# Kernel tuning notes

Measured on AMD Instinct MI355X. Metric: run time of the kernel, lower is better.

## Reference

```python
import jax, jax.numpy as jnp
import numpy as np

H = W = 128  # fixed by the hardcoded `127 - idx` in the original module


def _gather(x, gx, gy):
    # x: (B, H, W, C); gx, gy: (B, H, W) -> gathered (B, H, W, C)
    b = jnp.arange(x.shape[0])[:, None, None]
    return x[b, gx, gy]


def setup_inputs() -> dict:
    key = jax.random.key(0)
    k1, k2, k3 = jax.random.split(key, 3)
    B, C = 32, 64
    x1 = jax.random.normal(k1, (B, C, H, W), dtype=jnp.float32)
    x2 = jax.random.normal(k2, (B, C, H, W), dtype=jnp.float32)
    # 5 per-sample random bits: flipX, flipY, swap, flipX, flipY
    flip_bits = jax.random.randint(k3, (5, B), 0, 2, dtype=jnp.int32)
    return {"x1": x1, "x2": x2, "flip_bits": flip_bits}


def reference(x1, x2, flip_bits):
    B = x1.shape[0]
    x = jnp.concatenate([x1, x2], axis=1)            # (B, C_tot, H, W)
    x = jnp.transpose(x, (0, 2, 3, 1))               # NHWC for channel-last gather
    gx = jnp.broadcast_to(jnp.arange(H)[None, :, None], (B, H, W))
    gy = jnp.broadcast_to(jnp.arange(W)[None, None, :], (B, H, W))
    f = flip_bits[:, :, None, None].astype(bool)     # (5, B, 1, 1)
    # flipX
    x = _gather(x, jnp.where(f[0], (H - 1) - gx, gx), gy)
    # flipY
    x = _gather(x, gx, jnp.where(f[1], (W - 1) - gy, gy))
    # swap (transpose H/W indices per sample)
    x = _gather(x, jnp.where(f[2], gy, gx), jnp.where(f[2], gx, gy))
    # flipX
    x = _gather(x, jnp.where(f[3], (H - 1) - gx, gx), gy)
    # flipY
    x = _gather(x, gx, jnp.where(f[4], (W - 1) - gy, gy))
    x = jnp.transpose(x, (0, 3, 1, 2))               # back to NCHW
    c1 = x1.shape[1]
    return x[:, :c1], x[:, c1:]
```

## Files before the change

### kernel.cpp

```cpp
#include <hip/hip_runtime.h>


#define HWDIM  128
#define BCNT   32
#define CHALF  64
#define NF4    (HWDIM * HWDIM / 4)
#define PASSES (NF4 / 256)

__global__ __launch_bounds__(256, 2) void shuffle_aug_kernel(
    const float* __restrict__ x1,
    const float* __restrict__ x2,
    const int*   __restrict__ flips,
    float*       __restrict__ out)
{
    __shared__ float4 lds4[NF4];

    const int bid = blockIdx.x;
    const int ct  = bid & 127;
    const int b   = bid >> 7;

    const int f0 = flips[0 * BCNT + b];
    const int f1 = flips[1 * BCNT + b];
    const int f2 = flips[2 * BCNT + b];
    const int f3 = flips[3 * BCNT + b];
    const int f4 = flips[4 * BCNT + b];

    int sI = f3 ? -1 : 1, tI = f3 ? 127 : 0;
    int sJ = f4 ? -1 : 1, tJ = f4 ? 127 : 0;
    int sA, tA, sC, tC;
    if (f2) {
        sA = f0 ? -sJ : sJ;  tA = f0 ? 127 - tJ : tJ;
        sC = f1 ? -sI : sI;  tC = f1 ? 127 - tI : tI;
    } else {
        sA = f0 ? -sI : sI;  tA = f0 ? 127 - tI : tI;
        sC = f1 ? -sJ : sJ;  tC = f1 ? 127 - tJ : tJ;
    }

    const int cLoc = ct & (CHALF - 1);
    const size_t plane = (size_t)(b * CHALF + cLoc) * (HWDIM * HWDIM);
    const float4* __restrict__ src4 =
        reinterpret_cast<const float4*>(((ct < CHALF) ? x1 : x2) + plane);
    float4* __restrict__ dst4 = reinterpret_cast<float4*>(
        out + ((ct < CHALF) ? (size_t)0 : (size_t)BCNT * CHALF * HWDIM * HWDIM) + plane);

    const int t = threadIdx.x;
    const bool revA = ((f2 ? (f0 ^ f4) : (f0 ^ f3)) != 0);
    const bool revC = ((f2 ? (f1 ^ f3) : (f1 ^ f4)) != 0);
    (void)sA; (void)tA; (void)sC; (void)tC;

    if (!f2) {
#pragma unroll
        for (int p = 0; p < PASSES; ++p) {
            const int d   = p * 256 + t;
            const int i   = d >> 5, jf4 = d & 31;
            const int a   = revA ? (127 - i)  : i;
            const int cf4 = revC ? (31 - jf4) : jf4;
            float4 v = src4[(a << 5) | cf4];
            if (revC) { float x = v.x; v.x = v.w; v.w = x;
                        float y = v.y; v.y = v.z; v.z = y; }
            dst4[d] = v;
        }
    } else {
        float4 stage[PASSES];
#pragma unroll
        for (int p = 0; p < PASSES; ++p) stage[p] = src4[p * 256 + t];
#pragma unroll
        for (int p = 0; p < PASSES; ++p) {
            const int d = p * 256 + t;
            const int r = d >> 5, c4 = d & 31;
            lds4[(r << 5) | (c4 ^ ((r >> 2) & 31))] = stage[p];
        }
        __syncthreads();

        const float* __restrict__ ldsf = reinterpret_cast<const float*>(lds4);
#pragma unroll
        for (int p = 0; p < PASSES; ++p) {
            const int d = p * 256 + t;
            const int i = d >> 5, jf4 = d & 31;
            const int c  = revC ? (127 - i) : i;
            const int ch = c >> 2, ce = c & 3;
            float ov[4];
#pragma unroll
            for (int e = 0; e < 4; ++e) {
                const int j = 4 * jf4 + e;
                const int a = revA ? (127 - j) : j;
                ov[e] = ldsf[(((a << 5) | (ch ^ ((a >> 2) & 31))) << 2) + ce];
            }
            dst4[d] = make_float4(ov[0], ov[1], ov[2], ov[3]);
        }
    }
}

extern "C" void kernel_launch(void* const* d_in, const int* in_sizes, int n_in,
                              void* d_out, int out_size, void* d_ws, size_t ws_size,
                              hipStream_t stream) {
    const float* x1    = (const float*)d_in[0];
    const float* x2    = (const float*)d_in[1];
    const int*   flips = (const int*)d_in[2];
    float*       out   = (float*)d_out;

    const int grid = BCNT * 2 * CHALF;
    shuffle_aug_kernel<<<grid, 256, 0, stream>>>(x1, x2, flips, out);
}
```

Measured before the change: 437.5 us.

## Split each plane into 64x64 tiles with padded LDS transpose

Each 128x128 plane is now processed by four blocks, each owning a 64x64 output tile, which quadruples the grid and cuts LDS per block from 64KB to about 16KB. The swap path now uses a padded float array in place of the XOR-swizzled float4 layout. The aim is higher occupancy and more memory-level parallelism for this bandwidth-bound permutation. In exchange, the LDS writes become scalar, and the per-block flip setup is repeated across four times as many blocks.

```diff
diff --git a/kernel.cpp b/kernel.cpp
--- a/kernel.cpp
+++ b/kernel.cpp
@@ -4,20 +4,20 @@
 #define HWDIM  128
 #define BCNT   32
 #define CHALF  64
-#define NF4    (HWDIM * HWDIM / 4)
-#define PASSES (NF4 / 256)
+#define TILE   64
 
-__global__ __launch_bounds__(256, 2) void shuffle_aug_kernel(
+__global__ __launch_bounds__(256) void shuffle_aug_kernel(
     const float* __restrict__ x1,
     const float* __restrict__ x2,
     const int*   __restrict__ flips,
     float*       __restrict__ out)
 {
-    __shared__ float4 lds4[NF4];
+    __shared__ float lds[TILE][TILE + 1];
 
-    const int bid = blockIdx.x;
-    const int ct  = bid & 127;
-    const int b   = bid >> 7;
+    const int bid  = blockIdx.x;
+    const int tile = bid & 3;
+    const int ct   = (bid >> 2) & 127;
+    const int b    = bid >> 9;
 
     const int f0 = flips[0 * BCNT + b];
     const int f1 = flips[1 * BCNT + b];
@@ -25,16 +25,12 @@
     const int f3 = flips[3 * BCNT + b];
     const int f4 = flips[4 * BCNT + b];
 
-    int sI = f3 ? -1 : 1, tI = f3 ? 127 : 0;
-    int sJ = f4 ? -1 : 1, tJ = f4 ? 127 : 0;
-    int sA, tA, sC, tC;
-    if (f2) {
-        sA = f0 ? -sJ : sJ;  tA = f0 ? 127 - tJ : tJ;
-        sC = f1 ? -sI : sI;  tC = f1 ? 127 - tI : tI;
-    } else {
-        sA = f0 ? -sI : sI;  tA = f0 ? 127 - tI : tI;
-        sC = f1 ? -sJ : sJ;  tC = f1 ? 127 - tJ : tJ;
-    }
+    const bool swp  = (f2 != 0);
+    const bool revA = ((swp ? (f0 ^ f4) : (f0 ^ f3)) != 0);
+    const bool revC = ((swp ? (f1 ^ f3) : (f1 ^ f4)) != 0);
+
+    const int i0 = (tile >> 1) * TILE;
+    const int j0 = (tile & 1) * TILE;
 
     const int cLoc = ct & (CHALF - 1);
     const size_t plane = (size_t)(b * CHALF + cLoc) * (HWDIM * HWDIM);
@@ -44,49 +40,53 @@
         out + ((ct < CHALF) ? (size_t)0 : (size_t)BCNT * CHALF * HWDIM * HWDIM) + plane);
 
     const int t = threadIdx.x;
-    const bool revA = ((f2 ? (f0 ^ f4) : (f0 ^ f3)) != 0);
-    const bool revC = ((f2 ? (f1 ^ f3) : (f1 ^ f4)) != 0);
-    (void)sA; (void)tA; (void)sC; (void)tC;
 
-    if (!f2) {
+    if (!swp) {
 #pragma unroll
-        for (int p = 0; p < PASSES; ++p) {
+        for (int p = 0; p < 4; ++p) {
             const int d   = p * 256 + t;
-            const int i   = d >> 5, jf4 = d & 31;
-            const int a   = revA ? (127 - i)  : i;
-            const int cf4 = revC ? (31 - jf4) : jf4;
-            float4 v = src4[(a << 5) | cf4];
+            const int ir  = d >> 4;
+            const int jf4 = d & 15;
+            const int i   = i0 + ir;
+            const int a   = revA ? 127 - i : i;
+            const int cf4 = revC ? (31 - (j0 >> 2) - jf4) : ((j0 >> 2) + jf4);
+            float4 v = src4[a * 32 + cf4];
             if (revC) { float x = v.x; v.x = v.w; v.w = x;
                         float y = v.y; v.y = v.z; v.z = y; }
-            dst4[d] = v;
+            dst4[i * 32 + (j0 >> 2) + jf4] = v;
         }
     } else {
-        float4 stage[PASSES];
+        const int aMin = revA ? (TILE - j0) : j0;
+        const int cMin = revC ? (TILE - i0) : i0;
+
 #pragma unroll
-        for (int p = 0; p < PASSES; ++p) stage[p] = src4[p * 256 + t];
-#pragma unroll
-        for (int p = 0; p < PASSES; ++p) {
-            const int d = p * 256 + t;
-            const int r = d >> 5, c4 = d & 31;
-            lds4[(r << 5) | (c4 ^ ((r >> 2) & 31))] = stage[p];
+        for (int p = 0; p < 4; ++p) {
+            const int d  = p * 256 + t;
+            const int r  = d >> 4;
+            const int c4 = d & 15;
+            float4 v = src4[(aMin + r) * 32 + (cMin >> 2) + c4];
+            lds[r][c4 * 4 + 0] = v.x;
+            lds[r][c4 * 4 + 1] = v.y;
+            lds[r][c4 * 4 + 2] = v.z;
+            lds[r][c4 * 4 + 3] = v.w;
         }
         __syncthreads();
 
-        const float* __restrict__ ldsf = reinterpret_cast<const float*>(lds4);
 #pragma unroll
-        for (int p = 0; p < PASSES; ++p) {
-            const int d = p * 256 + t;
-            const int i = d >> 5, jf4 = d & 31;
-            const int c  = revC ? (127 - i) : i;
-            const int ch = c >> 2, ce = c & 3;
+        for (int p = 0; p < 4; ++p) {
+            const int d   = p * 256 + t;
+            const int ir  = d >> 4;
+            const int jf4 = d & 15;
+            const int i   = i0 + ir;
+            const int c   = (revC ? 127 - i : i) - cMin;
             float ov[4];
 #pragma unroll
             for (int e = 0; e < 4; ++e) {
-                const int j = 4 * jf4 + e;
-                const int a = revA ? (127 - j) : j;
-                ov[e] = ldsf[(((a << 5) | (ch ^ ((a >> 2) & 31))) << 2) + ce];
+                const int j = j0 + 4 * jf4 + e;
+                const int a = (revA ? 127 - j : j) - aMin;
+                ov[e] = lds[a][c];
             }
-            dst4[d] = make_float4(ov[0], ov[1], ov[2], ov[3]);
+            dst4[i * 32 + (j0 >> 2) + jf4] = make_float4(ov[0], ov[1], ov[2], ov[3]);
         }
     }
 }
@@ -99,6 +99,6 @@
     const int*   flips = (const int*)d_in[2];
     float*       out   = (float*)d_out;
 
-    const int grid = BCNT * 2 * CHALF;
+    const int grid = BCNT * 2 * CHALF * 4;
     shuffle_aug_kernel<<<grid, 256, 0, stream>>>(x1, x2, flips, out);
 }
```

Result: no change. 433.5 us (median of 2 runs) (-0.9%).
